# Kernel tuning notes

Hardware: AMD Instinct MI355X
Metric: run time of the kernel (lower is better)

## Reference

```python
import jax, jax.numpy as jnp
import numpy as np


def setup_inputs() -> dict:
    key = jax.random.key(0)
    ks = jax.random.split(key, 9)
    B, F, D = 512, 32, 64
    units = [128, 128, 128]
    inp = {
        "x": jax.random.normal(ks[0], (B, F, D), dtype=jnp.float32),
        "W0": jax.random.normal(ks[1], (units[0], F * F), dtype=jnp.float32) * 0.02,
        "b0": jax.random.normal(ks[2], (units[0],), dtype=jnp.float32) * 0.02,
        "W1": jax.random.normal(ks[3], (units[1], units[0] * F), dtype=jnp.float32) * 0.02,
        "b1": jax.random.normal(ks[4], (units[1],), dtype=jnp.float32) * 0.02,
        "W2": jax.random.normal(ks[5], (units[2], units[1] * F), dtype=jnp.float32) * 0.02,
        "b2": jax.random.normal(ks[6], (units[2],), dtype=jnp.float32) * 0.02,
        "Wout": jax.random.normal(ks[7], (sum(units), 1), dtype=jnp.float32) * 0.02,
        "bout": jax.random.normal(ks[8], (1,), dtype=jnp.float32) * 0.02,
    }
    return inp


def reference(x, W0, b0, W1, b1, W2, b2, Wout, bout):
    # x: [B, F, D]
    B, F, D = x.shape
    x0 = x[:, :, None, :]  # [B, F, 1, D]
    h = x                   # [B, H, D], H starts at F
    outs = []
    for W, b in ((W0, b0), (W1, b1), (W2, b2)):
        # outer product over field dims: [B, F, H, D]
        z = x0 * h[:, None, :, :]
        Bn, Fd, Hd, Dd = z.shape
        z = z.reshape(Bn, Fd * Hd, Dd)  # channels = f*H + h (torch view order)
        # 1x1 Conv1d == matmul over channels: [B, C_in, D] x [C_out, C_in]
        y = jnp.einsum('bcd,oc->bod', z, W) + b[None, :, None]  # [B, U, D]
        h = y
        outs.append(y.sum(axis=2))  # [B, U]
    out = jnp.concatenate(outs, axis=1)       # [B, sum(units)]
    out = jax.nn.relu(out)
    out = out @ Wout + bout                    # [B, 1]
    return jax.nn.sigmoid(out)
```

## Files before the change

kernel.cpp:

```cpp
#include <hip/hip_runtime.h>
#include <math.h>


typedef __attribute__((ext_vector_type(8))) _Float16 f16x8;
typedef __attribute__((ext_vector_type(4))) float f32x4;
typedef __attribute__((ext_vector_type(4))) unsigned short u16x4;

__device__ __forceinline__ unsigned short f2h(float f) {
  union { _Float16 h; unsigned short u; } c; c.h = (_Float16)f; return c.u;
}

__device__ __forceinline__ void gll16(const void* g, void* l) {
  __builtin_amdgcn_global_load_lds(
      (const __attribute__((address_space(1))) unsigned int*)g,
      (__attribute__((address_space(3))) unsigned int*)l, 16, 0, 0);
}

__global__ void repack_w_all(const float* __restrict__ W0q, const float* __restrict__ W1q,
                             const float* __restrict__ W2q,
                             unsigned short* __restrict__ D0, unsigned short* __restrict__ D1,
                             unsigned short* __restrict__ D2)
{
  const int blk = blockIdx.x;
  const float* W; unsigned short* dst; int H, t;
  if (blk < 64)       { W = W0q; dst = D0; H = 32;  t = blk * 256 + threadIdx.x; }
  else if (blk < 320) { W = W1q; dst = D1; H = 128; t = (blk - 64) * 256 + threadIdx.x; }
  else                { W = W2q; dst = D2; H = 128; t = (blk - 320) * 256 + threadIdx.x; }
  const int K = 32 * H;
  const int idx = t & 511;
  const int c   = t >> 9;
  const int pass = c >> 5, f = c & 31;
  const int mt = idx >> 6, l = idx & 63;
  const int o = mt * 16 + (l & 15);
  const int kcol = f * H + pass * 32 + ((l >> 4) & 3) * 8;
  const float* s = W + (size_t)o * K + kcol;
  u16x4 a, bq;
#pragma unroll
  for (int j = 0; j < 4; ++j) {
    a[j]  = f2h(s[j]);
    bq[j] = f2h(s[4 + j]);
  }
  *(u16x4*)(dst + (size_t)t * 8)     = a;
  *(u16x4*)(dst + (size_t)t * 8 + 4) = bq;
}

#define BODY(SPOFF, Ac, Ad, Ap)                                                 \
  {                                                                             \
    const float sc0 = lxp[(SPOFF) +  0 + li];                                   \
    const float sc1 = lxp[(SPOFF) + 16 + li];                                   \
    const float sc2 = lxp[(SPOFF) + 32 + li];                                   \
    const float sc3 = lxp[(SPOFF) + 48 + li];                                   \
    f32x4 G0, G1, G2, G3;                                                       \
    __builtin_amdgcn_s_setprio(1);                                              \
    G0 = __builtin_amdgcn_mfma_f32_16x16x32_f16(Ac, Bh[0], zero4, 0, 0, 0);     \
    G1 = __builtin_amdgcn_mfma_f32_16x16x32_f16(Ac, Bh[1], zero4, 0, 0, 0);     \
    G2 = __builtin_amdgcn_mfma_f32_16x16x32_f16(Ac, Bh[2], zero4, 0, 0, 0);     \
    G3 = __builtin_amdgcn_mfma_f32_16x16x32_f16(Ac, Bh[3], zero4, 0, 0, 0);     \
    __builtin_amdgcn_s_setprio(0);                                              \
    Ad = Ap[0];                                                                 \
    Ap += 1024;                                                                 \
    Y[0] += G0 * sc0;                                                           \
    Y[1] += G1 * sc1;                                                           \
    Y[2] += G2 * sc2;                                                           \
    Y[3] += G3 * sc3;                                                           \
  }

template<int H, int NPASS, bool FIRST, bool STORE_H, bool FINAL>
__global__ __launch_bounds__(512, 4) void cin_mfma_layer(
    const unsigned short* __restrict__ Wimg,
    const float* __restrict__ x,
    const unsigned short* __restrict__ hTin,
    const float* __restrict__ bias,
    unsigned short* __restrict__ hTout,
    float* __restrict__ outs, int col_off,
    const float* __restrict__ Wout,
    const float* __restrict__ bout,
    float* __restrict__ out)
{
  __shared__ char lds[8192];
  const int tid = threadIdx.x;
  const int w = tid >> 6, l = tid & 63, g = l >> 4, li = l & 15;
  const int b = blockIdx.x;
  const float* lx = (const float*)lds;

  gll16(x + (size_t)b * 2048 + tid * 4, lds + w * 1024);

  f32x4 Y[4];
#pragma unroll
  for (int nt = 0; nt < 4; ++nt) Y[nt] = (f32x4){0.f, 0.f, 0.f, 0.f};
  const f32x4 zero4 = (f32x4){0.f, 0.f, 0.f, 0.f};
  f16x8 Bh[4];

  asm volatile("s_waitcnt vmcnt(0)" ::: "memory");
  __builtin_amdgcn_s_barrier();

  if constexpr (FIRST) {
#pragma unroll
    for (int nt = 0; nt < 4; ++nt) {
      union { f16x8 v; _Float16 u[8]; } th;
#pragma unroll
      for (int j = 0; j < 8; ++j) {
        const float xv = lx[(g * 8 + j) * 64 + nt * 16 + li];
        th.u[j] = (_Float16)xv;
      }
      Bh[nt] = th.v;
    }
  }

  const f16x8* Abase = (const f16x8*)Wimg + (w * 64 + l);

  f16x8 Aa = Abase[0];
  f16x8 Ab = Abase[512];
  const f16x8* ApA = Abase + 1024;
  const f16x8* ApB = Abase + 1536;

  for (int pass = 0; pass < NPASS; ++pass) {
    if constexpr (!FIRST) {
#pragma unroll
      for (int nt = 0; nt < 4; ++nt) {
        const size_t off = (size_t)b * 8192 + (size_t)(nt * 16 + li) * 128
                         + pass * 32 + g * 8;
        Bh[nt] = *(const f16x8*)(hTin + off);
      }
    }
    const float* lxp = lx;
#pragma unroll 1
    for (int fo = 0; fo < 32; fo += 2) {
      BODY(0,  Aa, Aa, ApA)
      BODY(64, Ab, Ab, ApB)
      lxp += 128;
    }
  }

  const f32x4 bv = *(const f32x4*)(bias + w * 16 + g * 4);
#pragma unroll
  for (int nt = 0; nt < 4; ++nt) Y[nt] += bv;

  if constexpr (STORE_H) {
#pragma unroll
    for (int nt = 0; nt < 4; ++nt) {
      const int d = nt * 16 + li;
      u16x4 ph;
#pragma unroll
      for (int j = 0; j < 4; ++j) ph[j] = f2h(Y[nt][j]);
      const size_t off = (size_t)b * 8192 + (size_t)d * 128 + w * 16 + g * 4;
      *(u16x4*)(hTout + off) = ph;
    }
  }

  f32x4 s = Y[0] + Y[1] + Y[2] + Y[3];
#pragma unroll
  for (int m = 1; m < 16; m <<= 1) {
    s.x += __shfl_xor(s.x, m, 16);
    s.y += __shfl_xor(s.y, m, 16);
    s.z += __shfl_xor(s.z, m, 16);
    s.w += __shfl_xor(s.w, m, 16);
  }

  if constexpr (FINAL) {
    __builtin_amdgcn_s_barrier();
    float* shs = (float*)lds;
    if (li == 0) *(f32x4*)(shs + w * 16 + g * 4) = s;
    __builtin_amdgcn_s_barrier();
    if (w == 0) {
      float acc;
      {
        float v0 = shs[l];      v0 = v0 > 0.f ? v0 : 0.f;
        float v1 = shs[l + 64]; v1 = v1 > 0.f ? v1 : 0.f;
        acc = v0 * Wout[256 + l] + v1 * Wout[320 + l];
      }
#pragma unroll
      for (int q = 0; q < 4; ++q) {
        float v = outs[(size_t)b * 256 + q * 64 + l];
        v = v > 0.f ? v : 0.f;
        acc = fmaf(v, Wout[q * 64 + l], acc);
      }
#pragma unroll
      for (int m = 32; m; m >>= 1) acc += __shfl_xor(acc, m, 64);
      if (l == 0) {
        const float t = acc + bout[0];
        out[b] = 1.f / (1.f + expf(-t));
      }
    }
  } else {
    if (li == 0)
      *(f32x4*)(outs + (size_t)b * 256 + col_off + w * 16 + g * 4) = s;
  }
}

extern "C" void kernel_launch(void* const* d_in, const int* in_sizes, int n_in,
                              void* d_out, int out_size, void* d_ws, size_t ws_size,
                              hipStream_t stream)
{
  const float* x    = (const float*)d_in[0];
  const float* W0   = (const float*)d_in[1];
  const float* b0   = (const float*)d_in[2];
  const float* W1   = (const float*)d_in[3];
  const float* b1   = (const float*)d_in[4];
  const float* W2   = (const float*)d_in[5];
  const float* b2   = (const float*)d_in[6];
  const float* Wout = (const float*)d_in[7];
  const float* bout = (const float*)d_in[8];
  float* out = (float*)d_out;

  char* ws = (char*)d_ws;
  unsigned short* hT1  = (unsigned short*)ws;
  unsigned short* hT2  = (unsigned short*)(ws + (8 << 20));
  float*          outs = (float*)        (ws + (16 << 20));
  unsigned short* Wi0  = (unsigned short*)(ws + (17 << 20));
  unsigned short* Wi1  = (unsigned short*)(ws + (17 << 20) + (1 << 19));
  unsigned short* Wi2  = (unsigned short*)(ws + (19 << 20));

  repack_w_all<<<576, 256, 0, stream>>>(W0, W1, W2, Wi0, Wi1, Wi2);

  cin_mfma_layer<32,  1, true,  true,  false><<<512, 512, 0, stream>>>(
      Wi0, x, nullptr, b0, hT1, outs, 0, nullptr, nullptr, nullptr);
  cin_mfma_layer<128, 4, false, true,  false><<<512, 512, 0, stream>>>(
      Wi1, x, hT1, b1, hT2, outs, 128, nullptr, nullptr, nullptr);
  cin_mfma_layer<128, 4, false, false, true ><<<512, 512, 0, stream>>>(
      Wi2, x, hT2, b2, nullptr, outs, 0, Wout, bout, out);
}
```

Baseline: 106.5 us.

## Process two batch rows per block to reuse weight fragments across MFMAs

Each block now handles two batch elements, so every weight A-fragment loaded from global memory feeds eight MFMAs instead of four, halving weight traffic per sample. The x scalars are transposed into LDS so each lane fetches its four scale factors with one vector load instead of four scalar loads. Grid size is halved to 256 blocks and launch bounds are lowered to 2 blocks per SM to make room for the extra registers and 32KB of LDS. This costs occupancy and leaves only 256 blocks to fill the GPU.

```diff
diff --git a/kernel.cpp b/kernel.cpp
--- a/kernel.cpp
+++ b/kernel.cpp
@@ -46,27 +46,27 @@
 
 #define BODY(SPOFF, Ac, Ad, Ap)                                                 \
   {                                                                             \
-    const float sc0 = lxp[(SPOFF) +  0 + li];                                   \
-    const float sc1 = lxp[(SPOFF) + 16 + li];                                   \
-    const float sc2 = lxp[(SPOFF) + 32 + li];                                   \
-    const float sc3 = lxp[(SPOFF) + 48 + li];                                   \
-    f32x4 G0, G1, G2, G3;                                                       \
-    __builtin_amdgcn_s_setprio(1);                                              \
-    G0 = __builtin_amdgcn_mfma_f32_16x16x32_f16(Ac, Bh[0], zero4, 0, 0, 0);     \
-    G1 = __builtin_amdgcn_mfma_f32_16x16x32_f16(Ac, Bh[1], zero4, 0, 0, 0);     \
-    G2 = __builtin_amdgcn_mfma_f32_16x16x32_f16(Ac, Bh[2], zero4, 0, 0, 0);     \
-    G3 = __builtin_amdgcn_mfma_f32_16x16x32_f16(Ac, Bh[3], zero4, 0, 0, 0);     \
-    __builtin_amdgcn_s_setprio(0);                                              \
+    const f32x4 sv0 = *(const f32x4*)(lxp0 + (SPOFF));                          \
+    const f32x4 sv1 = *(const f32x4*)(lxp1 + (SPOFF));                          \
+    f32x4 G00, G01, G02, G03, G10, G11, G12, G13;                               \
+    G00 = __builtin_amdgcn_mfma_f32_16x16x32_f16(Ac, Bh0[0], zero4, 0, 0, 0);   \
+    G10 = __builtin_amdgcn_mfma_f32_16x16x32_f16(Ac, Bh1[0], zero4, 0, 0, 0);   \
+    G01 = __builtin_amdgcn_mfma_f32_16x16x32_f16(Ac, Bh0[1], zero4, 0, 0, 0);   \
+    G11 = __builtin_amdgcn_mfma_f32_16x16x32_f16(Ac, Bh1[1], zero4, 0, 0, 0);   \
+    G02 = __builtin_amdgcn_mfma_f32_16x16x32_f16(Ac, Bh0[2], zero4, 0, 0, 0);   \
+    G12 = __builtin_amdgcn_mfma_f32_16x16x32_f16(Ac, Bh1[2], zero4, 0, 0, 0);   \
+    G03 = __builtin_amdgcn_mfma_f32_16x16x32_f16(Ac, Bh0[3], zero4, 0, 0, 0);   \
+    G13 = __builtin_amdgcn_mfma_f32_16x16x32_f16(Ac, Bh1[3], zero4, 0, 0, 0);   \
     Ad = Ap[0];                                                                 \
     Ap += 1024;                                                                 \
-    Y[0] += G0 * sc0;                                                           \
-    Y[1] += G1 * sc1;                                                           \
-    Y[2] += G2 * sc2;                                                           \
-    Y[3] += G3 * sc3;                                                           \
+    Y0[0] += G00 * sv0[0];  Y0[1] += G01 * sv0[1];                              \
+    Y0[2] += G02 * sv0[2];  Y0[3] += G03 * sv0[3];                              \
+    Y1[0] += G10 * sv1[0];  Y1[1] += G11 * sv1[1];                              \
+    Y1[2] += G12 * sv1[2];  Y1[3] += G13 * sv1[3];                              \
   }
 
 template<int H, int NPASS, bool FIRST, bool STORE_H, bool FINAL>
-__global__ __launch_bounds__(512, 4) void cin_mfma_layer(
+__global__ __launch_bounds__(512, 2) void cin_mfma_layer(
     const unsigned short* __restrict__ Wimg,
     const float* __restrict__ x,
     const unsigned short* __restrict__ hTin,
@@ -77,38 +77,56 @@
     const float* __restrict__ bout,
     float* __restrict__ out)
 {
-  __shared__ char lds[8192];
+  __shared__ char lds[32768];
   const int tid = threadIdx.x;
   const int w = tid >> 6, l = tid & 63, g = l >> 4, li = l & 15;
-  const int b = blockIdx.x;
-  const float* lx = (const float*)lds;
-
-  gll16(x + (size_t)b * 2048 + tid * 4, lds + w * 1024);
-
-  f32x4 Y[4];
-#pragma unroll
-  for (int nt = 0; nt < 4; ++nt) Y[nt] = (f32x4){0.f, 0.f, 0.f, 0.f};
+  const int b0 = blockIdx.x * 2;
+  const float* lx0 = (const float*)lds;
+  const float* lx1 = (const float*)(lds + 8192);
+  const float* xt0 = (const float*)(lds + 16384);
+  const float* xt1 = (const float*)(lds + 24576);
+
+  gll16(x + (size_t)b0 * 2048 + tid * 4,       lds + w * 1024);
+  gll16(x + (size_t)(b0 + 1) * 2048 + tid * 4, lds + 8192 + w * 1024);
+
+  f32x4 Y0[4], Y1[4];
+#pragma unroll
+  for (int nt = 0; nt < 4; ++nt) {
+    Y0[nt] = (f32x4){0.f, 0.f, 0.f, 0.f};
+    Y1[nt] = (f32x4){0.f, 0.f, 0.f, 0.f};
+  }
   const f32x4 zero4 = (f32x4){0.f, 0.f, 0.f, 0.f};
-  f16x8 Bh[4];
+  f16x8 Bh0[4], Bh1[4];
 
   asm volatile("s_waitcnt vmcnt(0)" ::: "memory");
   __builtin_amdgcn_s_barrier();
 
+  {
+    const int tf = tid >> 4, tl = tid & 15;
+    f32x4 v0, v1;
+    v0[0] = lx0[tf * 64 +  0 + tl]; v0[1] = lx0[tf * 64 + 16 + tl];
+    v0[2] = lx0[tf * 64 + 32 + tl]; v0[3] = lx0[tf * 64 + 48 + tl];
+    v1[0] = lx1[tf * 64 +  0 + tl]; v1[1] = lx1[tf * 64 + 16 + tl];
+    v1[2] = lx1[tf * 64 + 32 + tl]; v1[3] = lx1[tf * 64 + 48 + tl];
+    *(f32x4*)(lds + 16384 + (tf * 16 + tl) * 16) = v0;
+    *(f32x4*)(lds + 24576 + (tf * 16 + tl) * 16) = v1;
+  }
+  __builtin_amdgcn_s_barrier();
+
   if constexpr (FIRST) {
 #pragma unroll
     for (int nt = 0; nt < 4; ++nt) {
-      union { f16x8 v; _Float16 u[8]; } th;
+      union { f16x8 v; _Float16 u[8]; } t0, t1;
 #pragma unroll
       for (int j = 0; j < 8; ++j) {
-        const float xv = lx[(g * 8 + j) * 64 + nt * 16 + li];
-        th.u[j] = (_Float16)xv;
-      }
-      Bh[nt] = th.v;
+        t0.u[j] = (_Float16)lx0[(g * 8 + j) * 64 + nt * 16 + li];
+        t1.u[j] = (_Float16)lx1[(g * 8 + j) * 64 + nt * 16 + li];
+      }
+      Bh0[nt] = t0.v; Bh1[nt] = t1.v;
     }
   }
 
   const f16x8* Abase = (const f16x8*)Wimg + (w * 64 + l);
-
   f16x8 Aa = Abase[0];
   f16x8 Ab = Abase[512];
   const f16x8* ApA = Abase + 1024;
@@ -118,60 +136,69 @@
     if constexpr (!FIRST) {
 #pragma unroll
       for (int nt = 0; nt < 4; ++nt) {
-        const size_t off = (size_t)b * 8192 + (size_t)(nt * 16 + li) * 128
-                         + pass * 32 + g * 8;
-        Bh[nt] = *(const f16x8*)(hTin + off);
-      }
-    }
-    const float* lxp = lx;
+        const size_t co = (size_t)(nt * 16 + li) * 128 + pass * 32 + g * 8;
+        Bh0[nt] = *(const f16x8*)(hTin + (size_t)b0 * 8192 + co);
+        Bh1[nt] = *(const f16x8*)(hTin + (size_t)(b0 + 1) * 8192 + co);
+      }
+    }
+    const float* lxp0 = xt0 + li * 4;
+    const float* lxp1 = xt1 + li * 4;
 #pragma unroll 1
     for (int fo = 0; fo < 32; fo += 2) {
       BODY(0,  Aa, Aa, ApA)
       BODY(64, Ab, Ab, ApB)
-      lxp += 128;
+      lxp0 += 128;
+      lxp1 += 128;
     }
   }
 
   const f32x4 bv = *(const f32x4*)(bias + w * 16 + g * 4);
 #pragma unroll
-  for (int nt = 0; nt < 4; ++nt) Y[nt] += bv;
+  for (int nt = 0; nt < 4; ++nt) { Y0[nt] += bv; Y1[nt] += bv; }
 
   if constexpr (STORE_H) {
 #pragma unroll
     for (int nt = 0; nt < 4; ++nt) {
       const int d = nt * 16 + li;
-      u16x4 ph;
-#pragma unroll
-      for (int j = 0; j < 4; ++j) ph[j] = f2h(Y[nt][j]);
-      const size_t off = (size_t)b * 8192 + (size_t)d * 128 + w * 16 + g * 4;
-      *(u16x4*)(hTout + off) = ph;
-    }
-  }
-
-  f32x4 s = Y[0] + Y[1] + Y[2] + Y[3];
+      u16x4 p0, p1;
+#pragma unroll
+      for (int j = 0; j < 4; ++j) { p0[j] = f2h(Y0[nt][j]); p1[j] = f2h(Y1[nt][j]); }
+      const size_t co = (size_t)d * 128 + w * 16 + g * 4;
+      *(u16x4*)(hTout + (size_t)b0 * 8192 + co)       = p0;
+      *(u16x4*)(hTout + (size_t)(b0 + 1) * 8192 + co) = p1;
+    }
+  }
+
+  f32x4 s0 = Y0[0] + Y0[1] + Y0[2] + Y0[3];
+  f32x4 s1 = Y1[0] + Y1[1] + Y1[2] + Y1[3];
 #pragma unroll
   for (int m = 1; m < 16; m <<= 1) {
-    s.x += __shfl_xor(s.x, m, 16);
-    s.y += __shfl_xor(s.y, m, 16);
-    s.z += __shfl_xor(s.z, m, 16);
-    s.w += __shfl_xor(s.w, m, 16);
+    s0.x += __shfl_xor(s0.x, m, 16); s0.y += __shfl_xor(s0.y, m, 16);
+    s0.z += __shfl_xor(s0.z, m, 16); s0.w += __shfl_xor(s0.w, m, 16);
+    s1.x += __shfl_xor(s1.x, m, 16); s1.y += __shfl_xor(s1.y, m, 16);
+    s1.z += __shfl_xor(s1.z, m, 16); s1.w += __shfl_xor(s1.w, m, 16);
   }
 
   if constexpr (FINAL) {
     __builtin_amdgcn_s_barrier();
     float* shs = (float*)lds;
-    if (li == 0) *(f32x4*)(shs + w * 16 + g * 4) = s;
+    if (li == 0) {
+      *(f32x4*)(shs + w * 16 + g * 4)       = s0;
+      *(f32x4*)(shs + 128 + w * 16 + g * 4) = s1;
+    }
     __builtin_amdgcn_s_barrier();
-    if (w == 0) {
+    if (w < 2) {
+      const int bb = b0 + w;
+      const float* sh = shs + w * 128;
       float acc;
       {
-        float v0 = shs[l];      v0 = v0 > 0.f ? v0 : 0.f;
-        float v1 = shs[l + 64]; v1 = v1 > 0.f ? v1 : 0.f;
+        float v0 = sh[l];      v0 = v0 > 0.f ? v0 : 0.f;
+        float v1 = sh[l + 64]; v1 = v1 > 0.f ? v1 : 0.f;
         acc = v0 * Wout[256 + l] + v1 * Wout[320 + l];
       }
 #pragma unroll
       for (int q = 0; q < 4; ++q) {
-        float v = outs[(size_t)b * 256 + q * 64 + l];
+        float v = outs[(size_t)bb * 256 + q * 64 + l];
         v = v > 0.f ? v : 0.f;
         acc = fmaf(v, Wout[q * 64 + l], acc);
       }
@@ -179,12 +206,14 @@
       for (int m = 32; m; m >>= 1) acc += __shfl_xor(acc, m, 64);
       if (l == 0) {
         const float t = acc + bout[0];
-        out[b] = 1.f / (1.f + expf(-t));
+        out[bb] = 1.f / (1.f + expf(-t));
       }
     }
   } else {
-    if (li == 0)
-      *(f32x4*)(outs + (size_t)b * 256 + col_off + w * 16 + g * 4) = s;
+    if (li == 0) {
+      *(f32x4*)(outs + (size_t)b0 * 256 + col_off + w * 16 + g * 4)       = s0;
+      *(f32x4*)(outs + (size_t)(b0 + 1) * 256 + col_off + w * 16 + g * 4) = s1;
+    }
   }
 }
 
@@ -213,10 +242,10 @@
 
   repack_w_all<<<576, 256, 0, stream>>>(W0, W1, W2, Wi0, Wi1, Wi2);
 
-  cin_mfma_layer<32,  1, true,  true,  false><<<512, 512, 0, stream>>>(
+  cin_mfma_layer<32,  1, true,  true,  false><<<256, 512, 0, stream>>>(
       Wi0, x, nullptr, b0, hT1, outs, 0, nullptr, nullptr, nullptr);
-  cin_mfma_layer<128, 4, false, true,  false><<<512, 512, 0, stream>>>(
+  cin_mfma_layer<128, 4, false, true,  false><<<256, 512, 0, stream>>>(
       Wi1, x, hT1, b1, hT2, outs, 128, nullptr, nullptr, nullptr);
-  cin_mfma_layer<128, 4, false, false, true ><<<512, 512, 0, stream>>>(
+  cin_mfma_layer<128, 4, false, false, true ><<<256, 512, 0, stream>>>(
       Wi2, x, hT2, b2, nullptr, outs, 0, Wout, bout, out);
 }
```

Measured after the change: 101.7 us. 1.05x faster.
